# Kernel tuning notes

Hardware: AMD Instinct MI355X
Metric: run time of the kernel (lower is better)

## Reference

```python
import jax, jax.numpy as jnp
import numpy as np

TEMPERATURE = 0.1
NEG_INF = -1e9
EPS = 1e-12

def setup_inputs() -> dict:
    key = jax.random.key(0)
    k1, k2, k3 = jax.random.split(key, 3)
    B, C, H, W = 8, 256, 128, 128
    num_classes = 150
    features = jax.random.normal(k1, (B, C, H, W), dtype=jnp.float32)
    labels = jax.random.randint(k2, (B, H, W), 0, num_classes, dtype=jnp.int32)
    text_embeddings = jax.random.normal(k3, (num_classes, C), dtype=jnp.float32)
    return {"features": features, "labels": labels, "text_embeddings": text_embeddings, "ignore_index": 255}

def _l2_normalize(x, axis=-1):
    n = jnp.linalg.norm(x, axis=axis, keepdims=True)
    return x / jnp.maximum(n, EPS)

def reference(features, labels, text_embeddings, ignore_index):
    num_classes, C = text_embeddings.shape
    B = features.shape[0]
    # [B,C,H,W] -> [B*H*W, C]
    f = jnp.transpose(features, (0, 2, 3, 1)).reshape(-1, C)
    lab = jnp.where(labels == ignore_index, 0, labels).reshape(-1)
    # segment-mean per class (fused scatter-add instead of per-class loop)
    sums = jax.ops.segment_sum(f, lab, num_segments=num_classes)          # [K,C]
    counts = jax.ops.segment_sum(jnp.ones_like(lab, dtype=f.dtype), lab, num_segments=num_classes)  # [K]
    valid = counts > 0
    prototypes = jnp.where(valid[:, None], sums / jnp.maximum(counts, 1.0)[:, None], 0.0)
    prototypes = _l2_normalize(prototypes)
    text_n = _l2_normalize(text_embeddings)
    sim = (prototypes @ text_n.T) / TEMPERATURE                            # [K,K]
    # cross-entropy restricted to valid rows/cols with identity soft targets
    masked = jnp.where(valid[None, :], sim, NEG_INF)                       # mask invalid cols
    logp = jax.nn.log_softmax(masked, axis=-1)
    diag = jnp.diagonal(logp)
    per_row = jnp.where(valid, -diag, 0.0)
    n_valid = jnp.sum(valid.astype(f.dtype))
    loss = jnp.sum(per_row) / jnp.maximum(n_valid, 1.0)
    return jnp.where(n_valid > 1, loss, 0.0)
```

## Files before the change

### kernel.cpp

```cpp
#include <hip/hip_runtime.h>
#include <math.h>

#define EPSV 1e-12f

typedef __attribute__((ext_vector_type(8))) short short8;
typedef __attribute__((ext_vector_type(4))) float f32x4;

constexpr int MT    = 10;
constexpr int K_PAD = MT * 16;
constexpr int CPB   = 64;
constexpr int CHUNK = 128;
constexpr int PBPX  = 1024;
constexpr int NCHK  = PBPX / CHUNK;
constexpr int NPB   = 128;
constexpr int THR   = 512;
constexpr int LROW  = 136;
constexpr int FROW  = 68;

__device__ __forceinline__ unsigned short f2bf(float f) {
    unsigned u = __builtin_bit_cast(unsigned, f);
    return (unsigned short)((u + 0x7FFFu + ((u >> 16) & 1u)) >> 16);
}

__global__ __launch_bounds__(THR, 4) void protomm_kernel(
    const float* __restrict__ feat,
    const int*   __restrict__ labels,
    const int*   __restrict__ ign_p,
    float*       __restrict__ partial,
    float*       __restrict__ vmask,
    int C, int HW)
{
    __shared__ unsigned short Bf[2][CPB * LROW];
    __shared__ int   labL[2][CHUNK];
    __shared__ float fscr[K_PAD * FROW];
    __shared__ unsigned char pres[K_PAD];

    const int tid   = threadIdx.x;
    const int w     = tid >> 6;
    const int l     = tid & 63;
    const int q     = w & 3;
    const int kh    = w >> 2;
    const int rowid = l & 15;
    const int g     = l >> 4;

    const int bid = blockIdx.x;
    const int cg  = bid & 3;
    const int pb  = bid >> 2;
    const int b   = pb >> 4;
    const int px0 = (pb & 15) * PBPX;
    const int ig  = *ign_p;

    const int qq  = tid & 31;
    const int chp = tid >> 5;
    const float* fb = feat + ((size_t)(b * C + cg * CPB + chp)) * HW + px0 + 4 * qq;
    const int*   lb = labels + (size_t)b * HW + px0;

    if (cg == 0)
        for (int i = tid; i < K_PAD; i += THR) pres[i] = 0;

    f32x4 acc[3][4];
    #pragma unroll
    for (int mi = 0; mi < 3; ++mi)
        #pragma unroll
        for (int ct = 0; ct < 4; ++ct)
            acc[mi][ct] = (f32x4){0.f, 0.f, 0.f, 0.f};

    float4 pf0, pf1, pf2, pf3;
    int4   plab;
    auto issue = [&](int ck) {
        const float* p = fb + ck * CHUNK;
        pf0 = *reinterpret_cast<const float4*>(p);
        pf1 = *reinterpret_cast<const float4*>(p + (size_t)16 * HW);
        pf2 = *reinterpret_cast<const float4*>(p + (size_t)32 * HW);
        pf3 = *reinterpret_cast<const float4*>(p + (size_t)48 * HW);
        if (tid < 32)
            plab = *reinterpret_cast<const int4*>(lb + ck * CHUNK + 4 * tid);
    };
    auto commit = [&](int buf) {
        float4 v[4] = {pf0, pf1, pf2, pf3};
        #pragma unroll
        for (int i = 0; i < 4; ++i) {
            unsigned* dst = reinterpret_cast<unsigned*>(
                &Bf[buf][(chp + 16 * i) * LROW + 4 * qq]);
            dst[0] = (unsigned)f2bf(v[i].x) | ((unsigned)f2bf(v[i].y) << 16);
            dst[1] = (unsigned)f2bf(v[i].z) | ((unsigned)f2bf(v[i].w) << 16);
        }
        if (tid < 32) {
            int4 lv = plab;
            lv.x = (lv.x == ig) ? 0 : lv.x;
            lv.y = (lv.y == ig) ? 0 : lv.y;
            lv.z = (lv.z == ig) ? 0 : lv.z;
            lv.w = (lv.w == ig) ? 0 : lv.w;
            *reinterpret_cast<int4*>(&labL[buf][4 * tid]) = lv;
        }
    };

    issue(0);

    for (int ck = 0; ck < NCHK; ++ck) {
        const int cur = ck & 1;
        commit(cur);
        if (ck + 1 < NCHK) issue(ck + 1);
        __syncthreads();

        if (cg == 0 && tid < CHUNK) {
            int la = labL[cur][tid];
            if ((unsigned)la < (unsigned)K_PAD) pres[la] = 1;
        }

        #pragma unroll
        for (int kk = 0; kk < 2; ++kk) {
            const int ks = 2 * kh + kk;
            const int4 lA = *reinterpret_cast<const int4*>(&labL[cur][ks * 32 + g * 8]);
            const int4 lB = *reinterpret_cast<const int4*>(&labL[cur][ks * 32 + g * 8 + 4]);
            short8 bfragv[4];
            #pragma unroll
            for (int ct = 0; ct < 4; ++ct)
                bfragv[ct] = *reinterpret_cast<const short8*>(
                    &Bf[cur][(ct * 16 + rowid) * LROW + ks * 32 + g * 8]);
            #pragma unroll
            for (int mi = 0; mi < 3; ++mi) {
                const int m = q + 4 * mi;
                if (m < MT) {
                    const int tgt = m * 16 + rowid;
                    unsigned w0 = (lA.x == tgt ? 0x3F80u : 0u) | (lA.y == tgt ? 0x3F800000u : 0u);
                    unsigned w1 = (lA.z == tgt ? 0x3F80u : 0u) | (lA.w == tgt ? 0x3F800000u : 0u);
                    unsigned w2 = (lB.x == tgt ? 0x3F80u : 0u) | (lB.y == tgt ? 0x3F800000u : 0u);
                    unsigned w3 = (lB.z == tgt ? 0x3F80u : 0u) | (lB.w == tgt ? 0x3F800000u : 0u);
                    uint4 aw = make_uint4(w0, w1, w2, w3);
                    short8 afrag = __builtin_bit_cast(short8, aw);
                    #pragma unroll
                    for (int ct = 0; ct < 4; ++ct)
                        acc[mi][ct] = __builtin_amdgcn_mfma_f32_16x16x32_bf16(
                            afrag, bfragv[ct], acc[mi][ct], 0, 0, 0);
                }
            }
        }
    }

    __syncthreads();
    if (kh == 1) {
        #pragma unroll
        for (int mi = 0; mi < 3; ++mi) {
            const int m = q + 4 * mi;
            if (m < MT)
                #pragma unroll
                for (int ct = 0; ct < 4; ++ct)
                    #pragma unroll
                    for (int r = 0; r < 4; ++r)
                        fscr[(m * 16 + g * 4 + r) * FROW + ct * 16 + rowid] = acc[mi][ct][r];
        }
    }
    __syncthreads();
    if (kh == 0) {
        float* dst = partial + (size_t)pb * K_PAD * C + cg * CPB;
        #pragma unroll
        for (int mi = 0; mi < 3; ++mi) {
            const int m = q + 4 * mi;
            if (m < MT)
                #pragma unroll
                for (int ct = 0; ct < 4; ++ct)
                    #pragma unroll
                    for (int r = 0; r < 4; ++r) {
                        const int cls = m * 16 + g * 4 + r;
                        const int col = ct * 16 + rowid;
                        dst[(size_t)cls * C + col] =
                            acc[mi][ct][r] + fscr[cls * FROW + col];
                    }
        }
    }
    if (cg == 0) {
        for (int i = tid; i < K_PAD; i += THR)
            if (pres[i]) vmask[i] = 1.0f;
    }
}

__global__ __launch_bounds__(256) void tail_kernel(
    const float* __restrict__ partial,
    const float* __restrict__ text,
    const float* __restrict__ vmask,
    float* __restrict__ loss_acc,
    unsigned int* __restrict__ ticket,
    float* __restrict__ out,
    int K, int C, int nblocks)
{
    __shared__ float ph[256];
    __shared__ float scr[4][260];
    __shared__ float vm[K_PAD];
    __shared__ float red[5];
    __shared__ float wred[12];
    __shared__ unsigned int lastflag;

    const int k    = blockIdx.x;
    const int tid  = threadIdx.x;
    const int wid  = tid >> 6;
    const int lane = tid & 63;

    if (tid < K_PAD) vm[tid] = vmask[tid];
    __syncthreads();
    const bool valid = (vm[k] > 0.f);

    float contrib = 0.f;
    if (valid) {
        const int cq = tid & 63;
        const int sg = tid >> 6;
        const size_t gs = (size_t)K_PAD * C;
        const float* pbase = partial + (size_t)k * C + 4 * cq;
        float4 a0 = {0,0,0,0}, a1 = {0,0,0,0}, a2 = {0,0,0,0}, a3 = {0,0,0,0};
        float4 a4 = {0,0,0,0}, a5 = {0,0,0,0}, a6 = {0,0,0,0}, a7 = {0,0,0,0};
        for (int s = sg; s < NPB; s += 32) {
            a0 += *(const float4*)(pbase + (size_t)(s +  0) * gs);
            a1 += *(const float4*)(pbase + (size_t)(s +  4) * gs);
            a2 += *(const float4*)(pbase + (size_t)(s +  8) * gs);
            a3 += *(const float4*)(pbase + (size_t)(s + 12) * gs);
            a4 += *(const float4*)(pbase + (size_t)(s + 16) * gs);
            a5 += *(const float4*)(pbase + (size_t)(s + 20) * gs);
            a6 += *(const float4*)(pbase + (size_t)(s + 24) * gs);
            a7 += *(const float4*)(pbase + (size_t)(s + 28) * gs);
        }
        float4 asum = (((a0 + a1) + (a2 + a3)) + ((a4 + a5) + (a6 + a7)));
        *(float4*)&scr[sg][4 * cq] = asum;
        __syncthreads();
        float val = scr[0][tid] + scr[1][tid] + scr[2][tid] + scr[3][tid];

        float v = val * val;
        #pragma unroll
        for (int o = 32; o > 0; o >>= 1) v += __shfl_down(v, o);
        if (lane == 0) red[wid] = v;
        __syncthreads();
        if (tid == 0) {
            float s = red[0] + red[1] + red[2] + red[3];
            red[4] = 1.0f / fmaxf(sqrtf(s), EPSV);
        }
        __syncthreads();
        ph[tid] = val * red[4];
        __syncthreads();

        const float4 pv = *(const float4*)&ph[4 * lane];
        float m = -INFINITY, s = 0.f, skk = 0.f;
        #pragma unroll 1
        for (int gq = 0; gq < K_PAD / 16; ++gq) {
            const int j0 = gq * 16 + wid * 4;
            const float4* t0 = (const float4*)(text + (size_t)(j0 + 0 < K ? j0 + 0 : 0) * C);
            const float4* t1 = (const float4*)(text + (size_t)(j0 + 1 < K ? j0 + 1 : 0) * C);
            const float4* t2 = (const float4*)(text + (size_t)(j0 + 2 < K ? j0 + 2 : 0) * C);
            const float4* t3 = (const float4*)(text + (size_t)(j0 + 3 < K ? j0 + 3 : 0) * C);
            float4 x0 = t0[lane], x1 = t1[lane], x2 = t2[lane], x3 = t3[lane];
            float d0 = pv.x*x0.x + pv.y*x0.y + pv.z*x0.z + pv.w*x0.w;
            float q0 = x0.x*x0.x + x0.y*x0.y + x0.z*x0.z + x0.w*x0.w;
            float d1 = pv.x*x1.x + pv.y*x1.y + pv.z*x1.z + pv.w*x1.w;
            float q1 = x1.x*x1.x + x1.y*x1.y + x1.z*x1.z + x1.w*x1.w;
            float d2 = pv.x*x2.x + pv.y*x2.y + pv.z*x2.z + pv.w*x2.w;
            float q2 = x2.x*x2.x + x2.y*x2.y + x2.z*x2.z + x2.w*x2.w;
            float d3 = pv.x*x3.x + pv.y*x3.y + pv.z*x3.z + pv.w*x3.w;
            float q3 = x3.x*x3.x + x3.y*x3.y + x3.z*x3.z + x3.w*x3.w;
            #pragma unroll
            for (int o = 32; o > 0; o >>= 1) {
                d0 += __shfl_down(d0, o); d1 += __shfl_down(d1, o);
                d2 += __shfl_down(d2, o); d3 += __shfl_down(d3, o);
                q0 += __shfl_down(q0, o); q1 += __shfl_down(q1, o);
                q2 += __shfl_down(q2, o); q3 += __shfl_down(q3, o);
            }
            if (lane == 0) {
                float dd[4] = {d0, d1, d2, d3};
                float qq[4] = {q0, q1, q2, q3};
                #pragma unroll
                for (int r = 0; r < 4; ++r) {
                    int j = j0 + r;
                    float vmj = (j < K_PAD) ? vm[j] : 0.f;
                    float sim = dd[r] * (10.0f / fmaxf(sqrtf(qq[r]), EPSV));
                    float ms  = vmj * sim - (1.f - vmj) * 1e9f;
                    if (j == k) skk = ms;
                    if (ms > m) { s = s * __expf(m - ms) + 1.f; m = ms; }
                    else        { s += __expf(ms - m); }
                }
            }
        }
        if (lane == 0) { wred[wid*3+0] = m; wred[wid*3+1] = s; wred[wid*3+2] = skk; }
        __syncthreads();
        if (tid == 0) {
            float M = fmaxf(fmaxf(wred[0], wred[3]), fmaxf(wred[6], wred[9]));
            float S = 0.f, SKK = 0.f;
            #pragma unroll
            for (int ww = 0; ww < 4; ++ww) {
                S   += wred[ww*3+1] * __expf(wred[ww*3+0] - M);
                SKK += wred[ww*3+2];
            }
            contrib = M + logf(S) - SKK;
        }
    }

    if (tid == 0) {
        if (valid) atomicAdd(loss_acc, contrib);
        __threadfence();
        unsigned old = atomicAdd(ticket, 1u);
        lastflag = (old == (unsigned)(nblocks - 1)) ? 1u : 0u;
    }
    __syncthreads();
    if (lastflag) {
        float v = (tid < K_PAD) ? vm[tid] : 0.f;
        #pragma unroll
        for (int o = 32; o > 0; o >>= 1) v += __shfl_down(v, o);
        if (lane == 0) red[wid] = v;
        __syncthreads();
        if (tid == 0) {
            float nv = red[0] + red[1] + red[2] + red[3];
            float total = atomicAdd(loss_acc, 0.0f);
            out[0] = (nv > 1.f) ? total / fmaxf(nv, 1.f) : 0.f;
        }
    }
}

extern "C" void kernel_launch(void* const* d_in, const int* in_sizes, int n_in,
                              void* d_out, int out_size, void* d_ws, size_t ws_size,
                              hipStream_t stream) {
    const float* feat   = (const float*)d_in[0];
    const int*   labels = (const int*)d_in[1];
    const float* text   = (const float*)d_in[2];
    const int*   ign    = (const int*)d_in[3];

    const int B  = 8;
    const int N  = in_sizes[1];
    const int HW = N / B;
    const int C  = in_sizes[0] / N;
    const int K  = in_sizes[2] / C;

    float*        partial  = (float*)d_ws;
    float*        vmask    = partial + (size_t)NPB * K_PAD * C;
    float*        loss_acc = vmask + K_PAD;
    unsigned int* ticket   = (unsigned int*)(loss_acc + 1);

    hipMemsetAsync(vmask, 0, (K_PAD + 2) * sizeof(float), stream);

    protomm_kernel<<<NPB * 4, THR, 0, stream>>>(
        feat, labels, ign, partial, vmask, C, HW);

    tail_kernel<<<K, 256, 0, stream>>>(
        partial, text, vmask, loss_acc, ticket, (float*)d_out, K, C, K);
}
```

Measured before the change: 66.32 us.

## Halve pixels per block and remap warps to channel tiles without LDS reduction

Pixels per block drop from 1024 to 512, which doubles the block count, and occupancy is raised to 8 blocks per CU. Warps are reassigned so each owns one channel tile and five class tiles over all K-steps, instead of splitting K across warp halves. This removes the fscr shared-memory cross-warp reduction and its barriers. The trade-off is twice as many partial buffers written to global memory and summed in the tail kernel, whose loop is changed to cover 256 partials.

```diff
diff --git a/kernel.cpp b/kernel.cpp
--- a/kernel.cpp
+++ b/kernel.cpp
@@ -10,19 +10,18 @@
 constexpr int K_PAD = MT * 16;
 constexpr int CPB   = 64;
 constexpr int CHUNK = 128;
-constexpr int PBPX  = 1024;
+constexpr int PBPX  = 512;
 constexpr int NCHK  = PBPX / CHUNK;
-constexpr int NPB   = 128;
+constexpr int NPB   = 256;
 constexpr int THR   = 512;
 constexpr int LROW  = 136;
-constexpr int FROW  = 68;
 
 __device__ __forceinline__ unsigned short f2bf(float f) {
     unsigned u = __builtin_bit_cast(unsigned, f);
     return (unsigned short)((u + 0x7FFFu + ((u >> 16) & 1u)) >> 16);
 }
 
-__global__ __launch_bounds__(THR, 4) void protomm_kernel(
+__global__ __launch_bounds__(THR, 8) void protomm_kernel(
     const float* __restrict__ feat,
     const int*   __restrict__ labels,
     const int*   __restrict__ ign_p,
@@ -32,22 +31,21 @@
 {
     __shared__ unsigned short Bf[2][CPB * LROW];
     __shared__ int   labL[2][CHUNK];
-    __shared__ float fscr[K_PAD * FROW];
     __shared__ unsigned char pres[K_PAD];
 
     const int tid   = threadIdx.x;
     const int w     = tid >> 6;
     const int l     = tid & 63;
-    const int q     = w & 3;
-    const int kh    = w >> 2;
+    const int ct    = w & 3;
+    const int par   = w >> 2;
     const int rowid = l & 15;
     const int g     = l >> 4;
 
     const int bid = blockIdx.x;
     const int cg  = bid & 3;
     const int pb  = bid >> 2;
-    const int b   = pb >> 4;
-    const int px0 = (pb & 15) * PBPX;
+    const int b   = pb >> 5;
+    const int px0 = (pb & 31) * PBPX;
     const int ig  = *ign_p;
 
     const int qq  = tid & 31;
@@ -58,12 +56,9 @@
     if (cg == 0)
         for (int i = tid; i < K_PAD; i += THR) pres[i] = 0;
 
-    f32x4 acc[3][4];
+    f32x4 acc[5];
     #pragma unroll
-    for (int mi = 0; mi < 3; ++mi)
-        #pragma unroll
-        for (int ct = 0; ct < 4; ++ct)
-            acc[mi][ct] = (f32x4){0.f, 0.f, 0.f, 0.f};
+    for (int j = 0; j < 5; ++j) acc[j] = (f32x4){0.f, 0.f, 0.f, 0.f};
 
     float4 pf0, pf1, pf2, pf3;
     int4   plab;
@@ -109,67 +104,39 @@
         }
 
         #pragma unroll
-        for (int kk = 0; kk < 2; ++kk) {
-            const int ks = 2 * kh + kk;
+        for (int ks = 0; ks < CHUNK / 32; ++ks) {
             const int4 lA = *reinterpret_cast<const int4*>(&labL[cur][ks * 32 + g * 8]);
             const int4 lB = *reinterpret_cast<const int4*>(&labL[cur][ks * 32 + g * 8 + 4]);
-            short8 bfragv[4];
+            const short8 bfrag = *reinterpret_cast<const short8*>(
+                &Bf[cur][(ct * 16 + rowid) * LROW + ks * 32 + g * 8]);
             #pragma unroll
-            for (int ct = 0; ct < 4; ++ct)
-                bfragv[ct] = *reinterpret_cast<const short8*>(
-                    &Bf[cur][(ct * 16 + rowid) * LROW + ks * 32 + g * 8]);
+            for (int j = 0; j < 5; ++j) {
+                const int tgt = (par + 2 * j) * 16 + rowid;
+                unsigned w0 = (lA.x == tgt ? 0x3F80u : 0u) | (lA.y == tgt ? 0x3F800000u : 0u);
+                unsigned w1 = (lA.z == tgt ? 0x3F80u : 0u) | (lA.w == tgt ? 0x3F800000u : 0u);
+                unsigned w2 = (lB.x == tgt ? 0x3F80u : 0u) | (lB.y == tgt ? 0x3F800000u : 0u);
+                unsigned w3 = (lB.z == tgt ? 0x3F80u : 0u) | (lB.w == tgt ? 0x3F800000u : 0u);
+                uint4 aw = make_uint4(w0, w1, w2, w3);
+                short8 afrag = __builtin_bit_cast(short8, aw);
+                acc[j] = __builtin_amdgcn_mfma_f32_16x16x32_bf16(afrag, bfrag, acc[j], 0, 0, 0);
+            }
+        }
+    }
+
+    {
+        float* dst = partial + (size_t)pb * K_PAD * C + cg * CPB + ct * 16 + rowid;
+        #pragma unroll
+        for (int j = 0; j < 5; ++j) {
+            const int m = par + 2 * j;
             #pragma unroll
-            for (int mi = 0; mi < 3; ++mi) {
-                const int m = q + 4 * mi;
-                if (m < MT) {
-                    const int tgt = m * 16 + rowid;
-                    unsigned w0 = (lA.x == tgt ? 0x3F80u : 0u) | (lA.y == tgt ? 0x3F800000u : 0u);
-                    unsigned w1 = (lA.z == tgt ? 0x3F80u : 0u) | (lA.w == tgt ? 0x3F800000u : 0u);
-                    unsigned w2 = (lB.x == tgt ? 0x3F80u : 0u) | (lB.y == tgt ? 0x3F800000u : 0u);
-                    unsigned w3 = (lB.z == tgt ? 0x3F80u : 0u) | (lB.w == tgt ? 0x3F800000u : 0u);
-                    uint4 aw = make_uint4(w0, w1, w2, w3);
-                    short8 afrag = __builtin_bit_cast(short8, aw);
-                    #pragma unroll
-                    for (int ct = 0; ct < 4; ++ct)
-                        acc[mi][ct] = __builtin_amdgcn_mfma_f32_16x16x32_bf16(
-                            afrag, bfragv[ct], acc[mi][ct], 0, 0, 0);
-                }
-            }
-        }
-    }
-
-    __syncthreads();
-    if (kh == 1) {
-        #pragma unroll
-        for (int mi = 0; mi < 3; ++mi) {
-            const int m = q + 4 * mi;
-            if (m < MT)
-                #pragma unroll
-                for (int ct = 0; ct < 4; ++ct)
-                    #pragma unroll
-                    for (int r = 0; r < 4; ++r)
-                        fscr[(m * 16 + g * 4 + r) * FROW + ct * 16 + rowid] = acc[mi][ct][r];
-        }
-    }
-    __syncthreads();
-    if (kh == 0) {
-        float* dst = partial + (size_t)pb * K_PAD * C + cg * CPB;
-        #pragma unroll
-        for (int mi = 0; mi < 3; ++mi) {
-            const int m = q + 4 * mi;
-            if (m < MT)
-                #pragma unroll
-                for (int ct = 0; ct < 4; ++ct)
-                    #pragma unroll
-                    for (int r = 0; r < 4; ++r) {
-                        const int cls = m * 16 + g * 4 + r;
-                        const int col = ct * 16 + rowid;
-                        dst[(size_t)cls * C + col] =
-                            acc[mi][ct][r] + fscr[cls * FROW + col];
-                    }
+            for (int r = 0; r < 4; ++r) {
+                const int cls = m * 16 + g * 4 + r;
+                dst[(size_t)cls * C] = acc[j][r];
+            }
         }
     }
     if (cg == 0) {
+        __syncthreads();
         for (int i = tid; i < K_PAD; i += THR)
             if (pres[i]) vmask[i] = 1.0f;
     }
@@ -208,15 +175,15 @@
         const float* pbase = partial + (size_t)k * C + 4 * cq;
         float4 a0 = {0,0,0,0}, a1 = {0,0,0,0}, a2 = {0,0,0,0}, a3 = {0,0,0,0};
         float4 a4 = {0,0,0,0}, a5 = {0,0,0,0}, a6 = {0,0,0,0}, a7 = {0,0,0,0};
-        for (int s = sg; s < NPB; s += 32) {
-            a0 += *(const float4*)(pbase + (size_t)(s +  0) * gs);
-            a1 += *(const float4*)(pbase + (size_t)(s +  4) * gs);
-            a2 += *(const float4*)(pbase + (size_t)(s +  8) * gs);
-            a3 += *(const float4*)(pbase + (size_t)(s + 12) * gs);
-            a4 += *(const float4*)(pbase + (size_t)(s + 16) * gs);
-            a5 += *(const float4*)(pbase + (size_t)(s + 20) * gs);
-            a6 += *(const float4*)(pbase + (size_t)(s + 24) * gs);
-            a7 += *(const float4*)(pbase + (size_t)(s + 28) * gs);
+        for (int o = 0; o < NPB; o += 32) {
+            a0 += *(const float4*)(pbase + (size_t)(o + sg +  0) * gs);
+            a1 += *(const float4*)(pbase + (size_t)(o + sg +  4) * gs);
+            a2 += *(const float4*)(pbase + (size_t)(o + sg +  8) * gs);
+            a3 += *(const float4*)(pbase + (size_t)(o + sg + 12) * gs);
+            a4 += *(const float4*)(pbase + (size_t)(o + sg + 16) * gs);
+            a5 += *(const float4*)(pbase + (size_t)(o + sg + 20) * gs);
+            a6 += *(const float4*)(pbase + (size_t)(o + sg + 24) * gs);
+            a7 += *(const float4*)(pbase + (size_t)(o + sg + 28) * gs);
         }
         float4 asum = (((a0 + a1) + (a2 + a3)) + ((a4 + a5) + (a6 + a7)));
         *(float4*)&scr[sg][4 * cq] = asum;
@@ -267,7 +234,7 @@
                 #pragma unroll
                 for (int r = 0; r < 4; ++r) {
                     int j = j0 + r;
-                    float vmj = (j < K_PAD) ? vm[j] : 0.f;
+                    float vmj = vm[j];
                     float sim = dd[r] * (10.0f / fmaxf(sqrtf(qq[r]), EPSV));
                     float ms  = vmj * sim - (1.f - vmj) * 1e9f;
                     if (j == k) skk = ms;
```

Result: slower. 114.8 us (+73.2%).
